# Performance work log

Measured on AMD Instinct MI355X. Metric: run time of the kernel, lower is better.

Reference implementation:

```python
import jax, jax.numpy as jnp
import numpy as np

N_NODES = 100000
N_EDGES = 1000000

def _gcn_conv(x, W, b, src, dst, n_nodes):
    # PyG GCNConv: linear first, then symmetric-normalized aggregation with self loops
    x = x @ W  # [N, F_out]
    loop = jnp.arange(n_nodes, dtype=src.dtype)
    src2 = jnp.concatenate([src, loop])
    dst2 = jnp.concatenate([dst, loop])
    deg = jax.ops.segment_sum(jnp.ones(src2.shape[0], x.dtype), dst2, num_segments=n_nodes)
    dinv = jnp.where(deg > 0, jax.lax.rsqrt(deg), 0.0)
    norm = dinv[src2] * dinv[dst2]  # [E+N]
    msgs = x[src2] * norm[:, None]  # gather + scale
    out = jax.ops.segment_sum(msgs, dst2, num_segments=n_nodes)  # scatter-add
    return out + b

def _pair_norm_si(x):
    # mode 'PN-SI', scale=1
    x = x - x.mean(axis=0)
    row_norm = jnp.sqrt(1e-6 + jnp.sum(x * x, axis=1, keepdims=True))
    return x / row_norm

def setup_inputs() -> dict:
    key = jax.random.key(0)
    k1, k2, k3, k4 = jax.random.split(key, 4)
    in_c, hid_c, out_c = 256, 64, 40
    x = jax.random.normal(k1, (N_NODES, in_c), dtype=jnp.float32)
    edge_index = jax.random.randint(k2, (2, N_EDGES), 0, N_NODES, dtype=jnp.int64)
    W1 = jax.random.normal(k3, (in_c, hid_c), dtype=jnp.float32) / np.sqrt(in_c)
    b1 = jnp.zeros((hid_c,), jnp.float32)
    W2 = jax.random.normal(k4, (hid_c, out_c), dtype=jnp.float32) / np.sqrt(hid_c)
    b2 = jnp.zeros((out_c,), jnp.float32)
    return {"x": x, "edge_index": edge_index, "W1": W1, "b1": b1, "W2": W2, "b2": b2}

def reference(x, edge_index, W1, b1, W2, b2):
    src, dst = edge_index[0], edge_index[1]
    n = x.shape[0]
    h = jax.nn.relu(_gcn_conv(x, W1, b1, src, dst, n))
    h = _gcn_conv(h, W2, b2, src, dst, n)
    h = _pair_norm_si(h)
    return jax.nn.log_softmax(h, axis=1)
```

## Files before the change

kernel.cpp:

```cpp
#include <hip/hip_runtime.h>
#include <hip/hip_fp16.h>
#include <math.h>

#define F_IN  256
#define F_HID 64
#define F_OUT 40
#define HS2_LD 64

typedef _Float16 h8 __attribute__((ext_vector_type(8)));
typedef _Float16 h4 __attribute__((ext_vector_type(4)));
typedef float f4 __attribute__((ext_vector_type(4)));

__global__ void k_degw(const int* __restrict__ dst, unsigned* __restrict__ degc, int E,
                       const float* __restrict__ W1, const float* __restrict__ W2,
                       __half* __restrict__ Wt, __half* __restrict__ W2t) {
    int i = blockIdx.x * 256 + threadIdx.x;
    if (i < E) {
        atomicAdd(&degc[dst[i]], 1u);
        return;
    }
    int j = i - E;
    if (j < 16384) {
        int k = j >> 6, n = j & 63;
        Wt[n * 256 + k] = __float2half(W1[j]);
    } else if (j < 20480) {
        int jj = j - 16384;
        int n = jj >> 6, k = jj & 63;
        W2t[n * 64 + k] = __float2half((n < F_OUT) ? W2[k * F_OUT + n] : 0.f);
    }
}

__global__ __launch_bounds__(256) void k_scan(const unsigned* __restrict__ degc,
                                              unsigned* __restrict__ aggf,
                                              unsigned* __restrict__ ticket,
                                              unsigned* __restrict__ rowptr,
                                              float* __restrict__ dinv,
                                              unsigned* __restrict__ cursor,
                                              float* __restrict__ colsum, int N) {
    __shared__ unsigned s[256];
    __shared__ unsigned sTick, sPfx, sTot;
    int tid = threadIdx.x;
    if (tid == 0) sTick = atomicAdd(ticket, 1u);
    if (blockIdx.x == 0 && tid < 64) colsum[tid] = 0.f;
    __syncthreads();
    unsigned b = sTick;
    int i = (int)b * 256 + tid;
    unsigned d = (i < N) ? degc[i] : 0u;
    unsigned v = (i < N) ? ((d + 8u) & ~7u) : 0u;
    s[tid] = v;
    __syncthreads();
    for (int off = 1; off < 256; off <<= 1) {
        unsigned t = (tid >= off) ? s[tid - off] : 0u;
        __syncthreads();
        s[tid] += t;
        __syncthreads();
    }
    unsigned incl = s[tid];
    if (tid == 255) {
        sTot = s[255];
        atomicExch(&aggf[b], s[255] | 0x40000000u);
    }
    __syncthreads();
    if (tid == 0) {
        unsigned run = 0;
        int pr = (int)b - 1;
        while (pr >= 0) {
            unsigned t;
            do { t = atomicAdd(&aggf[pr], 0u); } while ((t >> 30) == 0u);
            run += t & 0x3FFFFFFFu;
            if ((t >> 30) == 3u) break;
            --pr;
        }
        sPfx = run;
        atomicExch(&aggf[b], (run + sTot) | 0xC0000000u);
    }
    __syncthreads();
    unsigned pfx = sPfx;
    if (i < N) {
        rowptr[i] = pfx + incl - v;
        dinv[i] = rsqrtf((float)d + 1.0f);
        cursor[i] = 0u;
        if (i == N - 1) rowptr[N] = pfx + incl;
    }
    if (i == 0) dinv[N] = 1.0f;
}

__global__ void k_fillpad(const int* __restrict__ src, const int* __restrict__ dst,
                          const unsigned* __restrict__ degc,
                          const unsigned* __restrict__ rowptr, unsigned* __restrict__ cursor,
                          unsigned* __restrict__ colp, int E, int N) {
    int t = blockIdx.x * blockDim.x + threadIdx.x;
    if (t < E) {
        int d = dst[t];
        unsigned p = atomicAdd(&cursor[d], 1u);
        colp[rowptr[d] + p] = (unsigned)src[t];
    } else {
        int r = t - E;
        int i = r >> 3, j = r & 7;
        if (i < N) {
            unsigned d = degc[i];
            unsigned pd = (d + 8u) & ~7u;
            unsigned slot = d + (unsigned)j;
            if (slot < pd) colp[rowptr[i] + slot] = (j == 0) ? (unsigned)i : (unsigned)N;
        }
    }
}

#define XS 136
__global__ __launch_bounds__(256) void k_mm1(const float* __restrict__ x,
                                             const __half* __restrict__ Wth,
                                             const float* __restrict__ dinv,
                                             __half* __restrict__ hs1o, int N) {
    __shared__ _Float16 sX[64 * XS];
    const _Float16* Wt = (const _Float16*)Wth;
    _Float16* hs1 = (_Float16*)hs1o;
    int tid = threadIdx.x;
    int lane = tid & 63;
    int wv = tid >> 6;
    int m15 = lane & 15;
    int q = lane >> 4;
    int nbase = blockIdx.x * 64;

    h8 bf[8];
    #pragma unroll
    for (int kt = 0; kt < 8; ++kt)
        bf[kt] = *(const h8*)(Wt + (wv * 16 + m15) * 256 + kt * 32 + q * 8);

    f4 acc[4];
    #pragma unroll
    for (int mt = 0; mt < 4; ++mt) acc[mt] = (f4){0.f, 0.f, 0.f, 0.f};

    #pragma unroll
    for (int c = 0; c < 2; ++c) {
        #pragma unroll
        for (int p = 0; p < 8; ++p) {
            int idx = p * 256 + tid;
            int row = idx >> 5;
            int c4  = idx & 31;
            int node = nbase + row;
            float4 v = (node < N) ? *(const float4*)(x + (size_t)node * F_IN + c * 128 + c4 * 4)
                                  : make_float4(0.f, 0.f, 0.f, 0.f);
            h4 hv = { (_Float16)v.x, (_Float16)v.y, (_Float16)v.z, (_Float16)v.w };
            *(h4*)&sX[row * XS + c4 * 4] = hv;
        }
        __syncthreads();
        #pragma unroll
        for (int kt2 = 0; kt2 < 4; ++kt2) {
            #pragma unroll
            for (int mt = 0; mt < 4; ++mt) {
                h8 a = *(const h8*)&sX[(mt * 16 + m15) * XS + kt2 * 32 + q * 8];
                acc[mt] = __builtin_amdgcn_mfma_f32_16x16x32_f16(a, bf[c * 4 + kt2], acc[mt], 0, 0, 0);
            }
        }
        __syncthreads();
    }

    #pragma unroll
    for (int mt = 0; mt < 4; ++mt) {
        #pragma unroll
        for (int r = 0; r < 4; ++r) {
            int node = nbase + mt * 16 + q * 4 + r;
            if (node <= N) {
                float din = (node < N) ? dinv[node] : 1.0f;
                hs1[(size_t)node * F_HID + wv * 16 + m15] = (_Float16)(acc[mt][r] * din);
            }
        }
    }
}

__global__ __launch_bounds__(256) void k_agg1(const unsigned* __restrict__ rowptr,
                                              const unsigned* __restrict__ colp,
                                              const float* __restrict__ dinv,
                                              const __half* __restrict__ hs1o,
                                              const float* __restrict__ bias1,
                                              __half* __restrict__ agg1o, int N) {
    const _Float16* hp = (const _Float16*)hs1o;
    _Float16* agg1h = (_Float16*)agg1o;
    int lane = threadIdx.x & 63;
    int w = blockIdx.x * 4 + (threadIdx.x >> 6);
    int na = 2 * w, nb = 2 * w + 1;
    if (na >= N) return;
    int g = lane >> 3, c = lane & 7;

    float accA[8], accB[8];
    #pragma unroll
    for (int j = 0; j < 8; ++j) { accA[j] = 0.f; accB[j] = 0.f; }

    unsigned aE = rowptr[na], aEnd = rowptr[na + 1];
    bool hasB = (nb < N);
    unsigned bE = 0, bEnd = 0;
    if (hasB) { bE = rowptr[nb]; bEnd = rowptr[nb + 1]; }

    while (aE < aEnd && bE < bEnd) {
        unsigned sA = colp[aE + g];
        unsigned sB = colp[bE + g];
        h8 va = *(const h8*)(hp + (size_t)sA * F_HID + c * 8);
        h8 vb = *(const h8*)(hp + (size_t)sB * F_HID + c * 8);
        #pragma unroll
        for (int j = 0; j < 8; ++j) { accA[j] += (float)va[j]; accB[j] += (float)vb[j]; }
        aE += 8; bE += 8;
    }
    while (aE < aEnd) {
        unsigned sA = colp[aE + g];
        h8 va = *(const h8*)(hp + (size_t)sA * F_HID + c * 8);
        #pragma unroll
        for (int j = 0; j < 8; ++j) accA[j] += (float)va[j];
        aE += 8;
    }
    while (bE < bEnd) {
        unsigned sB = colp[bE + g];
        h8 vb = *(const h8*)(hp + (size_t)sB * F_HID + c * 8);
        #pragma unroll
        for (int j = 0; j < 8; ++j) accB[j] += (float)vb[j];
        bE += 8;
    }

    #pragma unroll
    for (int off = 8; off <= 32; off <<= 1) {
        #pragma unroll
        for (int j = 0; j < 8; ++j) {
            accA[j] += __shfl_xor(accA[j], off, 64);
            accB[j] += __shfl_xor(accB[j], off, 64);
        }
    }

    if (g == 0) {
        float bv[8];
        *(float4*)&bv[0] = *(const float4*)(bias1 + c * 8);
        *(float4*)&bv[4] = *(const float4*)(bias1 + c * 8 + 4);
        float dinA = dinv[na];
        h8 ho;
        #pragma unroll
        for (int j = 0; j < 8; ++j) ho[j] = (_Float16)fmaxf(accA[j] * dinA + bv[j], 0.f);
        *(h8*)(agg1h + (size_t)na * F_HID + c * 8) = ho;
        if (hasB) {
            float dinB = dinv[nb];
            #pragma unroll
            for (int j = 0; j < 8; ++j) ho[j] = (_Float16)fmaxf(accB[j] * dinB + bv[j], 0.f);
            *(h8*)(agg1h + (size_t)nb * F_HID + c * 8) = ho;
        }
    }
}

#define AS 72
__global__ __launch_bounds__(256) void k_mm2(const __half* __restrict__ agg1o,
                                             const __half* __restrict__ W2th,
                                             const float* __restrict__ dinv,
                                             __half* __restrict__ hs2o, int N) {
    __shared__ _Float16 sA[64 * AS];
    const _Float16* agg1h = (const _Float16*)agg1o;
    const _Float16* W2t = (const _Float16*)W2th;
    _Float16* hs2 = (_Float16*)hs2o;
    int tid = threadIdx.x;
    int lane = tid & 63;
    int wv = tid >> 6;
    int m15 = lane & 15;
    int q = lane >> 4;
    int nbase = blockIdx.x * 64;

    h8 bf[2];
    #pragma unroll
    for (int kt = 0; kt < 2; ++kt)
        bf[kt] = *(const h8*)(W2t + (wv * 16 + m15) * 64 + kt * 32 + q * 8);

    #pragma unroll
    for (int p = 0; p < 2; ++p) {
        int idx = p * 256 + tid;
        int row = idx >> 3;
        int c8  = idx & 7;
        int node = nbase + row;
        h8 v;
        if (node < N) v = *(const h8*)(agg1h + (size_t)node * F_HID + c8 * 8);
        else          v = (h8){0, 0, 0, 0, 0, 0, 0, 0};
        *(h8*)&sA[row * AS + c8 * 8] = v;
    }
    __syncthreads();

    f4 acc[4];
    #pragma unroll
    for (int mt = 0; mt < 4; ++mt) acc[mt] = (f4){0.f, 0.f, 0.f, 0.f};
    #pragma unroll
    for (int kt = 0; kt < 2; ++kt) {
        #pragma unroll
        for (int mt = 0; mt < 4; ++mt) {
            h8 a = *(const h8*)&sA[(mt * 16 + m15) * AS + kt * 32 + q * 8];
            acc[mt] = __builtin_amdgcn_mfma_f32_16x16x32_f16(a, bf[kt], acc[mt], 0, 0, 0);
        }
    }

    #pragma unroll
    for (int mt = 0; mt < 4; ++mt) {
        #pragma unroll
        for (int r = 0; r < 4; ++r) {
            int node = nbase + mt * 16 + q * 4 + r;
            if (node <= N) {
                float din = (node < N) ? dinv[node] : 1.0f;
                hs2[(size_t)node * HS2_LD + wv * 16 + m15] = (_Float16)(acc[mt][r] * din);
            }
        }
    }
}

__global__ __launch_bounds__(256) void k_agg2(const unsigned* __restrict__ rowptr,
                                              const unsigned* __restrict__ colp,
                                              const float* __restrict__ dinv,
                                              const __half* __restrict__ hs2o,
                                              float* __restrict__ out,
                                              float* __restrict__ colsum, int N) {
    __shared__ float part[4][8][8];
    const _Float16* hp = (const _Float16*)hs2o;
    int lane = threadIdx.x & 63;
    int wv = threadIdx.x >> 6;
    int g = lane >> 3, c = lane & 7;
    int nwaves = gridDim.x * 4;
    float csum[8];
    #pragma unroll
    for (int j = 0; j < 8; ++j) csum[j] = 0.f;

    for (int w = blockIdx.x * 4 + wv; 2 * w < N; w += nwaves) {
        int na = 2 * w, nb = 2 * w + 1;
        float accA[8], accB[8];
        #pragma unroll
        for (int j = 0; j < 8; ++j) { accA[j] = 0.f; accB[j] = 0.f; }

        unsigned aE = rowptr[na], aEnd = rowptr[na + 1];
        bool hasB = (nb < N);
        unsigned bE = 0, bEnd = 0;
        if (hasB) { bE = rowptr[nb]; bEnd = rowptr[nb + 1]; }

        while (aE < aEnd && bE < bEnd) {
            unsigned sA = colp[aE + g];
            unsigned sB = colp[bE + g];
            h8 va = *(const h8*)(hp + (size_t)sA * HS2_LD + c * 8);
            h8 vb = *(const h8*)(hp + (size_t)sB * HS2_LD + c * 8);
            #pragma unroll
            for (int j = 0; j < 8; ++j) { accA[j] += (float)va[j]; accB[j] += (float)vb[j]; }
            aE += 8; bE += 8;
        }
        while (aE < aEnd) {
            unsigned sA = colp[aE + g];
            h8 va = *(const h8*)(hp + (size_t)sA * HS2_LD + c * 8);
            #pragma unroll
            for (int j = 0; j < 8; ++j) accA[j] += (float)va[j];
            aE += 8;
        }
        while (bE < bEnd) {
            unsigned sB = colp[bE + g];
            h8 vb = *(const h8*)(hp + (size_t)sB * HS2_LD + c * 8);
            #pragma unroll
            for (int j = 0; j < 8; ++j) accB[j] += (float)vb[j];
            bE += 8;
        }

        #pragma unroll
        for (int off = 8; off <= 32; off <<= 1) {
            #pragma unroll
            for (int j = 0; j < 8; ++j) {
                accA[j] += __shfl_xor(accA[j], off, 64);
                accB[j] += __shfl_xor(accB[j], off, 64);
            }
        }

        if (g == 0) {
            float dinA = dinv[na];
            #pragma unroll
            for (int j = 0; j < 8; ++j) { accA[j] *= dinA; csum[j] += accA[j]; }
            if (c < 5) {
                *(float4*)(out + (size_t)na * F_OUT + c * 8) =
                    make_float4(accA[0], accA[1], accA[2], accA[3]);
                *(float4*)(out + (size_t)na * F_OUT + c * 8 + 4) =
                    make_float4(accA[4], accA[5], accA[6], accA[7]);
            }
            if (hasB) {
                float dinB = dinv[nb];
                #pragma unroll
                for (int j = 0; j < 8; ++j) { accB[j] *= dinB; csum[j] += accB[j]; }
                if (c < 5) {
                    *(float4*)(out + (size_t)nb * F_OUT + c * 8) =
                        make_float4(accB[0], accB[1], accB[2], accB[3]);
                    *(float4*)(out + (size_t)nb * F_OUT + c * 8 + 4) =
                        make_float4(accB[4], accB[5], accB[6], accB[7]);
                }
            }
        }
    }

    if (g == 0) {
        #pragma unroll
        for (int j = 0; j < 8; ++j) part[wv][c][j] = csum[j];
    }
    __syncthreads();
    int tid = threadIdx.x;
    if (tid < F_OUT) {
        int cc = tid >> 3, jj = tid & 7;
        float s = part[0][cc][jj] + part[1][cc][jj] + part[2][cc][jj] + part[3][cc][jj];
        atomicAdd(&colsum[tid], s);
    }
}

__global__ __launch_bounds__(128) void k_final(float* __restrict__ out,
                                               const float* __restrict__ colsum, int N) {
    __shared__ float sMean[F_OUT];
    if (threadIdx.x < F_OUT) sMean[threadIdx.x] = colsum[threadIdx.x] * (1.0f / (float)N);
    __syncthreads();
    int n = blockIdx.x * blockDim.x + threadIdx.x;
    if (n >= N) return;
    float* row = out + (size_t)n * F_OUT;
    float v[F_OUT];
    float ss = 0.f;
    #pragma unroll
    for (int f = 0; f < F_OUT; ++f) {
        float t = row[f] - sMean[f];
        v[f] = t;
        ss += t * t;
    }
    float scale = 1.0f / sqrtf(ss + 1e-6f);
    float m = -1e30f;
    #pragma unroll
    for (int f = 0; f < F_OUT; ++f) {
        float y = v[f] * scale;
        v[f] = y;
        m = fmaxf(m, y);
    }
    float sum = 0.f;
    #pragma unroll
    for (int f = 0; f < F_OUT; ++f) sum += expf(v[f] - m);
    float lse = logf(sum);
    #pragma unroll
    for (int f = 0; f < F_OUT; ++f) row[f] = v[f] - m - lse;
}

extern "C" void kernel_launch(void* const* d_in, const int* in_sizes, int n_in,
                              void* d_out, int out_size, void* d_ws, size_t ws_size,
                              hipStream_t stream) {
    const float* x  = (const float*)d_in[0];
    const int*   ei = (const int*)d_in[1];
    const float* W1 = (const float*)d_in[2];
    const float* b1 = (const float*)d_in[3];
    const float* W2 = (const float*)d_in[4];
    float* out = (float*)d_out;

    int N = in_sizes[0] / F_IN;
    int E = in_sizes[1] / 2;
    const int* src = ei;
    const int* dst = ei + E;

    char* p = (char*)d_ws;
    auto alloc = [&](size_t bytes) { char* r = p; p += (bytes + 127) & ~(size_t)127; return r; };
    unsigned* degc   = (unsigned*)alloc((size_t)N * 4);
    unsigned* aggf   = (unsigned*)alloc(512 * 4);
    unsigned* ticket = (unsigned*)alloc(4);
    char* zend = p;
    unsigned* cursor = (unsigned*)alloc((size_t)N * 4);
    float*    colsum = (float*)   alloc(64 * 4);
    unsigned* rowptr = (unsigned*)alloc((size_t)(N + 1) * 4);
    unsigned* colp   = (unsigned*)alloc((size_t)(E + 8 * N + 8) * 4);
    float*    dinv   = (float*)   alloc((size_t)(N + 1) * 4);
    __half*   agg1h  = (__half*)  alloc((size_t)64 * (N + 1) * 2);
    __half*   hs1    = (__half*)  alloc((size_t)64 * (N + 1) * 2);
    __half*   hs2    = (__half*)  alloc((size_t)64 * (N + 1) * 2);
    __half*   Wt     = (__half*)  alloc((size_t)16384 * 2);
    __half*   W2t    = (__half*)  alloc((size_t)4096 * 2);

    hipMemsetAsync(d_ws, 0, (size_t)(zend - (char*)d_ws), stream);

    int nA = (N + 255) / 256;
    k_degw<<<(E + 20480 + 255) / 256, 256, 0, stream>>>(dst, degc, E, W1, W2, Wt, W2t);
    k_scan<<<nA, 256, 0, stream>>>(degc, aggf, ticket, rowptr, dinv, cursor, colsum, N);
    k_fillpad<<<(E + 8 * N + 255) / 256, 256, 0, stream>>>(src, dst, degc, rowptr, cursor, colp, E, N);
    k_mm1<<<(N + 63) / 64, 256, 0, stream>>>(x, Wt, dinv, hs1, N);
    int waves1 = (N + 1) / 2;
    k_agg1<<<(waves1 + 3) / 4, 256, 0, stream>>>(rowptr, colp, dinv, hs1, b1, agg1h, N);
    k_mm2<<<(N + 64) / 64, 256, 0, stream>>>(agg1h, W2t, dinv, hs2, N);
    k_agg2<<<2048, 256, 0, stream>>>(rowptr, colp, dinv, hs2, out, colsum, N);
    k_final<<<(N + 127) / 128, 128, 0, stream>>>(out, colsum, N);
}
```

Before: 402.8 us.

## Partition CSR fill by destination range and drop LDS staging in mm1

The CSR fill kernel now runs a fixed 2048-block grid. Each group of blocks scans the whole edge list and keeps only edges whose destination falls in one of eight node ranges, so the atomics and colp writes for a range stay clustered. The price is reading dst eight times over. Separately, the first GEMM now has each wave load its 16 x rows straight from global memory into MFMA operands, converting in registers and reading W1 tiles per k-step. This removes the shared-memory staging and both barriers but drops the LDS-based reuse of x across waves.

```diff
diff --git a/kernel.cpp b/kernel.cpp
--- a/kernel.cpp
+++ b/kernel.cpp
@@ -85,33 +85,38 @@
     if (i == 0) dinv[N] = 1.0f;
 }
 
-__global__ void k_fillpad(const int* __restrict__ src, const int* __restrict__ dst,
+__global__ __launch_bounds__(256) void k_fillpad(const int* __restrict__ src, const int* __restrict__ dst,
                           const unsigned* __restrict__ degc,
                           const unsigned* __restrict__ rowptr, unsigned* __restrict__ cursor,
                           unsigned* __restrict__ colp, int E, int N) {
-    int t = blockIdx.x * blockDim.x + threadIdx.x;
-    if (t < E) {
+    int r  = blockIdx.x & 7;
+    int sb = blockIdx.x >> 3;
+    int S  = gridDim.x >> 3;
+    int lo = (int)(((long long)N * r) >> 3);
+    int hi = (int)(((long long)N * (r + 1)) >> 3);
+    int tid = threadIdx.x;
+    int stride = S * 256;
+    for (int t = sb * 256 + tid; t < E; t += stride) {
         int d = dst[t];
-        unsigned p = atomicAdd(&cursor[d], 1u);
-        colp[rowptr[d] + p] = (unsigned)src[t];
-    } else {
-        int r = t - E;
-        int i = r >> 3, j = r & 7;
-        if (i < N) {
-            unsigned d = degc[i];
-            unsigned pd = (d + 8u) & ~7u;
-            unsigned slot = d + (unsigned)j;
-            if (slot < pd) colp[rowptr[i] + slot] = (j == 0) ? (unsigned)i : (unsigned)N;
-        }
-    }
-}
-
-#define XS 136
+        if (d >= lo && d < hi) {
+            unsigned p = atomicAdd(&cursor[d], 1u);
+            colp[rowptr[d] + p] = (unsigned)src[t];
+        }
+    }
+    int npad = (hi - lo) * 8;
+    for (int z = sb * 256 + tid; z < npad; z += stride) {
+        int i = lo + (z >> 3), j = z & 7;
+        unsigned d = degc[i];
+        unsigned slot = d + (unsigned)j;
+        if (slot < ((d + 8u) & ~7u))
+            colp[rowptr[i] + slot] = (j == 0) ? (unsigned)i : (unsigned)N;
+    }
+}
+
 __global__ __launch_bounds__(256) void k_mm1(const float* __restrict__ x,
                                              const __half* __restrict__ Wth,
                                              const float* __restrict__ dinv,
                                              __half* __restrict__ hs1o, int N) {
-    __shared__ _Float16 sX[64 * XS];
     const _Float16* Wt = (const _Float16*)Wth;
     _Float16* hs1 = (_Float16*)hs1o;
     int tid = threadIdx.x;
@@ -119,50 +124,42 @@
     int wv = tid >> 6;
     int m15 = lane & 15;
     int q = lane >> 4;
-    int nbase = blockIdx.x * 64;
-
-    h8 bf[8];
-    #pragma unroll
-    for (int kt = 0; kt < 8; ++kt)
-        bf[kt] = *(const h8*)(Wt + (wv * 16 + m15) * 256 + kt * 32 + q * 8);
+    int node0 = blockIdx.x * 64 + wv * 16;
+    int arow = node0 + m15;
+    bool ok = (arow < N);
+    const float* xr = x + (size_t)arow * F_IN + q * 8;
 
     f4 acc[4];
     #pragma unroll
-    for (int mt = 0; mt < 4; ++mt) acc[mt] = (f4){0.f, 0.f, 0.f, 0.f};
-
-    #pragma unroll
-    for (int c = 0; c < 2; ++c) {
-        #pragma unroll
-        for (int p = 0; p < 8; ++p) {
-            int idx = p * 256 + tid;
-            int row = idx >> 5;
-            int c4  = idx & 31;
-            int node = nbase + row;
-            float4 v = (node < N) ? *(const float4*)(x + (size_t)node * F_IN + c * 128 + c4 * 4)
-                                  : make_float4(0.f, 0.f, 0.f, 0.f);
-            h4 hv = { (_Float16)v.x, (_Float16)v.y, (_Float16)v.z, (_Float16)v.w };
-            *(h4*)&sX[row * XS + c4 * 4] = hv;
-        }
-        __syncthreads();
-        #pragma unroll
-        for (int kt2 = 0; kt2 < 4; ++kt2) {
-            #pragma unroll
-            for (int mt = 0; mt < 4; ++mt) {
-                h8 a = *(const h8*)&sX[(mt * 16 + m15) * XS + kt2 * 32 + q * 8];
-                acc[mt] = __builtin_amdgcn_mfma_f32_16x16x32_f16(a, bf[c * 4 + kt2], acc[mt], 0, 0, 0);
-            }
-        }
-        __syncthreads();
-    }
-
-    #pragma unroll
-    for (int mt = 0; mt < 4; ++mt) {
-        #pragma unroll
-        for (int r = 0; r < 4; ++r) {
-            int node = nbase + mt * 16 + q * 4 + r;
+    for (int nt = 0; nt < 4; ++nt) acc[nt] = (f4){0.f, 0.f, 0.f, 0.f};
+
+    #pragma unroll
+    for (int kt = 0; kt < 8; ++kt) {
+        float4 v0, v1;
+        if (ok) {
+            v0 = *(const float4*)(xr + kt * 32);
+            v1 = *(const float4*)(xr + kt * 32 + 4);
+        } else {
+            v0 = make_float4(0.f, 0.f, 0.f, 0.f);
+            v1 = v0;
+        }
+        h8 a = { (_Float16)v0.x, (_Float16)v0.y, (_Float16)v0.z, (_Float16)v0.w,
+                 (_Float16)v1.x, (_Float16)v1.y, (_Float16)v1.z, (_Float16)v1.w };
+        #pragma unroll
+        for (int nt = 0; nt < 4; ++nt) {
+            h8 b = *(const h8*)(Wt + (nt * 16 + m15) * 256 + kt * 32 + q * 8);
+            acc[nt] = __builtin_amdgcn_mfma_f32_16x16x32_f16(a, b, acc[nt], 0, 0, 0);
+        }
+    }
+
+    #pragma unroll
+    for (int nt = 0; nt < 4; ++nt) {
+        #pragma unroll
+        for (int rr = 0; rr < 4; ++rr) {
+            int node = node0 + q * 4 + rr;
             if (node <= N) {
                 float din = (node < N) ? dinv[node] : 1.0f;
-                hs1[(size_t)node * F_HID + wv * 16 + m15] = (_Float16)(acc[mt][r] * din);
+                hs1[(size_t)node * F_HID + nt * 16 + m15] = (_Float16)(acc[nt][rr] * din);
             }
         }
     }
@@ -467,7 +464,7 @@
     int nA = (N + 255) / 256;
     k_degw<<<(E + 20480 + 255) / 256, 256, 0, stream>>>(dst, degc, E, W1, W2, Wt, W2t);
     k_scan<<<nA, 256, 0, stream>>>(degc, aggf, ticket, rowptr, dinv, cursor, colsum, N);
-    k_fillpad<<<(E + 8 * N + 255) / 256, 256, 0, stream>>>(src, dst, degc, rowptr, cursor, colp, E, N);
+    k_fillpad<<<2048, 256, 0, stream>>>(src, dst, degc, rowptr, cursor, colp, E, N);
     k_mm1<<<(N + 63) / 64, 256, 0, stream>>>(x, Wt, dinv, hs1, N);
     int waves1 = (N + 1) / 2;
     k_agg1<<<(waves1 + 3) / 4, 256, 0, stream>>>(rowptr, colp, dinv, hs1, b1, agg1h, N);
```

Result: faster. 393.9 us (-2.2%).
